# Kernel optimization log

Hardware: AMD Instinct MI355X
Metric: run time of the kernel (lower is better)

The kernel has to match this reference:

```python
import jax, jax.numpy as jnp
import numpy as np

N = 100000   # nodes
E = 800000   # directed edges (symmetrized to 2E in forward)
D0 = 128     # input feature dim (dim0)
H = 128      # hidden = h_dim * args.d = 64 * 2
L = 4        # num_layers
G = 64       # num graphs for global_mean_pool
BN_EPS = 1e-5
LN_EPS = 1e-5


def setup_inputs() -> dict:
    key = jax.random.key(0)
    ks = jax.random.split(key, 12)
    s = 1.0 / np.sqrt(H)
    x = jax.random.normal(ks[0], (N, D0), dtype=jnp.float32)
    row = jax.random.randint(ks[1], (E,), 0, N, dtype=jnp.int32)
    off = jax.random.randint(ks[2], (E,), 1, N, dtype=jnp.int32)
    col = (row + off) % N  # guarantees row != col (no self loops)
    edge_index = jnp.stack([row, col])
    batch = jnp.sort(jax.random.randint(ks[3], (N,), 0, G, dtype=jnp.int32))
    return {
        "x": x,
        "W0": jax.random.normal(ks[4], (D0, H), dtype=jnp.float32) * s,
        "b0": jnp.zeros((H,), jnp.float32),
        "eps_l": jnp.zeros((L,), jnp.float32),        # GIN eps per layer
        "W1": jax.random.normal(ks[5], (L, H, H), dtype=jnp.float32) * s,
        "b1": jnp.zeros((L, H), jnp.float32),
        "bn_g": jnp.ones((L, H), jnp.float32),
        "bn_b": jnp.zeros((L, H), jnp.float32),
        "W2": jax.random.normal(ks[6], (L, H, H), dtype=jnp.float32) * s,
        "b2": jnp.zeros((L, H), jnp.float32),
        "ln_g": jnp.ones((L, H), jnp.float32),
        "ln_b": jnp.zeros((L, H), jnp.float32),
        "edge_index": edge_index,
        "batch": batch,
    }


def reference(x, W0, b0, eps_l, W1, b1, bn_g, bn_b, W2, b2, ln_g, ln_b, edge_index, batch):
    n = x.shape[0]
    h = x @ W0 + b0  # layer0 encode -> [N, H]
    # FNSD: symmetrize edges (cat with flip) and drop self loops
    ei = jnp.concatenate([edge_index, edge_index[::-1]], axis=1)
    row, col = ei[0], ei[1]
    w = (row != col).astype(h.dtype)  # self-loop removal as zero edge weight
    for i in range(L):
        # GINConv: scatter-add of neighbor features
        agg = jax.ops.segment_sum(w[:, None] * h[col], row, num_segments=n)
        u = (1.0 + eps_l[i]) * h + agg
        # mlp: Linear -> BatchNorm1d (training-mode batch stats) -> ReLU -> Linear
        z = u @ W1[i] + b1[i]
        m = jnp.mean(z, axis=0)
        v = jnp.var(z, axis=0)
        z = (z - m) * jax.lax.rsqrt(v + BN_EPS) * bn_g[i] + bn_b[i]
        z = jax.nn.relu(z)
        z = z @ W2[i] + b2[i]
        z = jax.nn.relu(z)          # use_activation
        h = h + z                    # use_residual
        mu = jnp.mean(h, axis=-1, keepdims=True)   # LayerNorm
        var = jnp.var(h, axis=-1, keepdims=True)
        h = (h - mu) * jax.lax.rsqrt(var + LN_EPS) * ln_g[i] + ln_b[i]
    # global_mean_pool over graph ids
    cnt = jax.ops.segment_sum(jnp.ones((n,), h.dtype), batch, num_segments=G)
    sums = jax.ops.segment_sum(h, batch, num_segments=G)
    return sums / jnp.maximum(cnt, 1.0)[:, None]
```

## Files before the change

kernel.cpp:

```cpp
#include <hip/hip_runtime.h>

#define NN 100000
#define EE 800000
#define HH 128
#define LL 4
#define GG 64
#define BN_EPS 1e-5f
#define LN_EPS 1e-5f
#define POOL_CHUNK 64
#define NBUK ((NN + 255) >> 8)
#define CAP 8192
#define BCHUNK 8192

typedef __attribute__((ext_vector_type(8))) short short8;
typedef __attribute__((ext_vector_type(4))) float f32x4;

__device__ inline unsigned short bf16_rne(float f) {
    unsigned u = __float_as_uint(f);
    return (unsigned short)((u + 0x7FFF + ((u >> 16) & 1)) >> 16);
}
__device__ inline float bf16_to_f32(unsigned short h) {
    return __uint_as_float((unsigned)h << 16);
}


__global__ void setup_kernel(const float* __restrict__ W0, const float* __restrict__ W1,
                             const float* __restrict__ W2, short* __restrict__ wt_hi,
                             int* __restrict__ bcur, float* __restrict__ colsum,
                             float* __restrict__ psum, float* __restrict__ pcnt) {
    int i = blockIdx.x * 256 + threadIdx.x;
    if (i < NBUK) bcur[i] = i * CAP;
    if (i < LL * HH * 2) colsum[i] = 0.f;
    if (i < GG * HH) psum[i] = 0.f;
    if (i < GG) pcnt[i] = 0.f;
    if (i < 9 * HH * HH) {
        int mat = i >> 14, rem = i & 16383;
        int n = rem >> 7, k = rem & 127;
        const float* src = (mat == 0) ? W0 : ((mat <= 4) ? W1 + (size_t)(mat - 1) * HH * HH
                                                         : W2 + (size_t)(mat - 5) * HH * HH);
        float v = src[(size_t)k * HH + n];
        int off = (mat << 14) + (((k >> 3) * 8 + (n >> 4)) << 7) + ((n & 15) << 3) + (k & 7);
        wt_hi[off] = (short)bf16_rne(v);
    }
}


__global__ __launch_bounds__(256) void bucket_scatter(const int* __restrict__ ei, int* __restrict__ bcur,
                                                      int* __restrict__ pairs) {
    __shared__ int h[NBUK];
    __shared__ int curb[NBUK];
    int tid = threadIdx.x;
    for (int i = tid; i < NBUK; i += 256) h[i] = 0;
    __syncthreads();
    int base = blockIdx.x * BCHUNK;
#pragma unroll 4
    for (int k = 0; k < BCHUNK / 256; k++) {
        int e = base + k * 256 + tid;
        if (e < 2 * EE) {
            int r = ei[e];
            int c = (e < EE) ? ei[e + EE] : ei[e - EE];
            if (r != c) atomicAdd(&h[r >> 8], 1);
        }
    }
    __syncthreads();
    for (int i = tid; i < NBUK; i += 256) {
        int n = h[i];
        curb[i] = n ? atomicAdd(&bcur[i], n) : 0;
    }
    __syncthreads();
#pragma unroll 4
    for (int k = 0; k < BCHUNK / 256; k++) {
        int e = base + k * 256 + tid;
        if (e < 2 * EE) {
            int r = ei[e];
            int c = (e < EE) ? ei[e + EE] : ei[e - EE];
            if (r != c) {
                int p = atomicAdd(&curb[r >> 8], 1);
                pairs[p] = ((r & 255) << 17) | c;
            }
        }
    }
}

__global__ __launch_bounds__(256) void bucket_build(const int* __restrict__ pairs, const int* __restrict__ bcur,
                                                    int* __restrict__ rp, int* __restrict__ re,
                                                    int* __restrict__ colidx) {
    __shared__ int hist[256], off[256], lcol[CAP];
    int b = blockIdx.x, tid = threadIdx.x;
    int s = b * CAP;
    int size = bcur[b] - s;
    hist[tid] = 0;
    __syncthreads();
    for (int i = tid; i < size; i += 256) atomicAdd(&hist[pairs[s + i] >> 17], 1);
    __syncthreads();
    off[tid] = hist[tid];
    __syncthreads();
    for (int o = 1; o < 256; o <<= 1) {
        int x = (tid >= o) ? off[tid - o] : 0;
        __syncthreads();
        off[tid] += x;
        __syncthreads();
    }
    int excl = (tid > 0) ? off[tid - 1] : 0;
    int r = (b << 8) + tid;
    if (r < NN) { rp[r] = s + excl; re[r] = s + off[tid]; }
    hist[tid] = excl;
    __syncthreads();
    for (int i = tid; i < size; i += 256) {
        int u = pairs[s + i];
        int p = atomicAdd(&hist[u >> 17], 1);
        lcol[p] = u & 0x1FFFF;
    }
    __syncthreads();
    for (int i = tid; i < size; i += 256) colidx[s + i] = lcol[i];
}


__global__ __launch_bounds__(256) void agg_kernel(
    const unsigned int* __restrict__ hbf, const int* __restrict__ rp, const int* __restrict__ re,
    const int* __restrict__ colidx,
    const float* __restrict__ eps_l, int layer, float* __restrict__ u)
{
    int node = blockIdx.x * 4 + (threadIdx.x >> 6);
    if (node >= NN) return;
    int lane = threadIdx.x & 63;
    float eps1 = 1.0f + eps_l[layer];
    unsigned sv = hbf[node * 64 + lane];
    float ax = __uint_as_float(sv << 16) * eps1;
    float ay = __uint_as_float(sv & 0xFFFF0000u) * eps1;
    int i = rp[node], end = re[node];
    for (; i + 8 <= end; i += 8) {
        unsigned v[8];
#pragma unroll
        for (int j = 0; j < 8; j++) v[j] = hbf[colidx[i + j] * 64 + lane];
#pragma unroll
        for (int j = 0; j < 8; j++) {
            ax += __uint_as_float(v[j] << 16);
            ay += __uint_as_float(v[j] & 0xFFFF0000u);
        }
    }
    for (; i + 2 <= end; i += 2) {
        unsigned v0 = hbf[colidx[i] * 64 + lane];
        unsigned v1 = hbf[colidx[i + 1] * 64 + lane];
        ax += __uint_as_float(v0 << 16) + __uint_as_float(v1 << 16);
        ay += __uint_as_float(v0 & 0xFFFF0000u) + __uint_as_float(v1 & 0xFFFF0000u);
    }
    for (; i < end; i++) {
        unsigned v = hbf[colidx[i] * 64 + lane];
        ax += __uint_as_float(v << 16);
        ay += __uint_as_float(v & 0xFFFF0000u);
    }
    ((float2*)(u + (size_t)node * HH))[lane] = make_float2(ax, ay);
}


template<int MODE>
__global__ __launch_bounds__(256, 4) void gemm_v8(
    const void* __restrict__ Ain,
    const short* __restrict__ wt_hi,
    const float* __restrict__ bias,
    unsigned short* __restrict__ z1_out,
    float* __restrict__ colsum, float* __restrict__ colsq,
    const float* __restrict__ bng, const float* __restrict__ bnb,
    const float* __restrict__ lng, const float* __restrict__ lnb,
    unsigned short* __restrict__ hbf)
{
    __shared__ short wh[HH * HH];
    __shared__ float stats[2 * HH];
    int tid = threadIdx.x;
    int wave = tid >> 6, lane = tid & 63;
    int lrow = lane & 15, kgrp = lane >> 4;
    int r0 = blockIdx.x * 64;
    int arow = r0 + wave * 16 + lrow;

    {
        const short8* src = (const short8*)wt_hi;
        short8* dst = (short8*)wh;
#pragma unroll
        for (int i = 0; i < 8; i++) dst[tid + i * 256] = src[tid + i * 256];
    }
    if (MODE == 1) stats[tid] = 0.f;
    if (MODE == 2 && tid < HH) {
        float m = colsum[tid] * (1.f / NN);
        float v = colsq[tid] * (1.f / NN) - m * m;
        float a = bng[tid] * rsqrtf(v + BN_EPS);
        stats[tid] = a;
        stats[HH + tid] = bnb[tid] - m * a;
    }

    float4 a0[4], a1[4];
    short8 az[4];
    if (MODE == 2) {
        const unsigned short* Az = (const unsigned short*)Ain;
        if (arow < NN) {
#pragma unroll
            for (int ks = 0; ks < 4; ks++)
                az[ks] = *(const short8*)(Az + (size_t)arow * HH + ks * 32 + kgrp * 8);
        } else {
#pragma unroll
            for (int ks = 0; ks < 4; ks++) az[ks] = (short8){0,0,0,0,0,0,0,0};
        }
    } else {
        const float* Af = (const float*)Ain;
        if (arow < NN) {
#pragma unroll
            for (int ks = 0; ks < 4; ks++) {
                int kb = ks * 32 + kgrp * 8;
                a0[ks] = *(const float4*)(Af + (size_t)arow * HH + kb);
                a1[ks] = *(const float4*)(Af + (size_t)arow * HH + kb + 4);
            }
        } else {
#pragma unroll
            for (int ks = 0; ks < 4; ks++) {
                a0[ks] = make_float4(0.f, 0.f, 0.f, 0.f);
                a1[ks] = a0[ks];
            }
        }
    }
    __syncthreads();

    f32x4 acc[8];
#pragma unroll
    for (int c = 0; c < 8; c++) acc[c] = (f32x4){0.f, 0.f, 0.f, 0.f};

#pragma unroll
    for (int ks = 0; ks < 4; ks++) {
        int kb = ks * 32 + kgrp * 8;
        float av[8];
        if (MODE == 2) {
#pragma unroll
            for (int j = 0; j < 8; j++) {
                float zb = bf16_to_f32((unsigned short)az[ks][j]);
                av[j] = fmaxf(fmaf(zb, stats[kb + j], stats[HH + kb + j]), 0.f);
            }
        } else {
            av[0] = a0[ks].x; av[1] = a0[ks].y; av[2] = a0[ks].z; av[3] = a0[ks].w;
            av[4] = a1[ks].x; av[5] = a1[ks].y; av[6] = a1[ks].z; av[7] = a1[ks].w;
        }
        short8 ahi, alo;
#pragma unroll
        for (int j = 0; j < 8; j++) {
            unsigned short hb = bf16_rne(av[j]);
            ahi[j] = (short)hb;
            alo[j] = (short)bf16_rne(av[j] - bf16_to_f32(hb));
        }
        int fb = (ks * 4 + kgrp) * 8;
#pragma unroll
        for (int c = 0; c < 8; c++) {
            short8 whi = *(const short8*)(wh + ((fb + c) << 7) + (lrow << 3));
            acc[c] = __builtin_amdgcn_mfma_f32_16x16x32_bf16(ahi, whi, acc[c], 0, 0, 0);
            acc[c] = __builtin_amdgcn_mfma_f32_16x16x32_bf16(alo, whi, acc[c], 0, 0, 0);
        }
    }

    float bv[8];
#pragma unroll
    for (int c = 0; c < 8; c++) bv[c] = bias[c * 16 + lrow];
    int lrb = wave * 16 + kgrp * 4;
    unsigned short* hst = (unsigned short*)wh;

    if (MODE == 0) {
        __syncthreads();
#pragma unroll
        for (int c = 0; c < 8; c++)
#pragma unroll
            for (int reg = 0; reg < 4; reg++)
                hst[(lrb + reg) * HH + c * 16 + lrow] = bf16_rne(acc[c][reg] + bv[c]);
        __syncthreads();
#pragma unroll
        for (int i = 0; i < 4; i++) {
            int idx = tid + i * 256;
            int r = r0 + (idx >> 4);
            if (r < NN)
                *(uint4*)(hbf + (size_t)r * HH + (idx & 15) * 8) = ((const uint4*)wh)[idx];
        }
    } else if (MODE == 1) {
        __syncthreads();
        float ps[8], pq[8];
#pragma unroll
        for (int c = 0; c < 8; c++) { ps[c] = 0.f; pq[c] = 0.f; }
#pragma unroll
        for (int c = 0; c < 8; c++)
#pragma unroll
            for (int reg = 0; reg < 4; reg++) {
                float z = acc[c][reg] + bv[c];
                hst[(lrb + reg) * HH + c * 16 + lrow] = bf16_rne(z);
                if (r0 + lrb + reg < NN) { ps[c] += z; pq[c] += z * z; }
            }
#pragma unroll
        for (int c = 0; c < 8; c++) {
            ps[c] += __shfl_xor(ps[c], 16); pq[c] += __shfl_xor(pq[c], 16);
            ps[c] += __shfl_xor(ps[c], 32); pq[c] += __shfl_xor(pq[c], 32);
        }
        if (kgrp == 0) {
#pragma unroll
            for (int c = 0; c < 8; c++) {
                atomicAdd(&stats[c * 16 + lrow], ps[c]);
                atomicAdd(&stats[HH + c * 16 + lrow], pq[c]);
            }
        }
        __syncthreads();
#pragma unroll
        for (int i = 0; i < 4; i++) {
            int idx = tid + i * 256;
            int r = r0 + (idx >> 4);
            if (r < NN)
                *(uint4*)(z1_out + (size_t)r * HH + (idx & 15) * 8) = ((const uint4*)wh)[idx];
        }
        if (tid < HH) {
            atomicAdd(&colsum[tid], stats[tid]);
            atomicAdd(&colsq[tid], stats[HH + tid]);
        }
    } else {
        float lg[8], lb[8];
#pragma unroll
        for (int c = 0; c < 8; c++) {
            lg[c] = lng[c * 16 + lrow];
            lb[c] = lnb[c * 16 + lrow];
        }
        __syncthreads();
#pragma unroll
        for (int i = 0; i < 4; i++) {
            int idx = tid + i * 256;
            int r = r0 + (idx >> 4);
            uint4 v = make_uint4(0, 0, 0, 0);
            if (r < NN) v = *(const uint4*)(hbf + (size_t)r * HH + (idx & 15) * 8);
            ((uint4*)wh)[idx] = v;
        }
        __syncthreads();
#pragma unroll
        for (int reg = 0; reg < 4; reg++) {
            int r = r0 + lrb + reg;
            if (r < NN) {
                float tv[8];
                float s = 0.f, q = 0.f;
#pragma unroll
                for (int c = 0; c < 8; c++) {
                    float hold = bf16_to_f32(hst[(lrb + reg) * HH + c * 16 + lrow]);
                    tv[c] = hold + fmaxf(acc[c][reg] + bv[c], 0.f);
                    s += tv[c]; q += tv[c] * tv[c];
                }
#pragma unroll
                for (int m = 1; m < 16; m <<= 1) {
                    s += __shfl_xor(s, m);
                    q += __shfl_xor(q, m);
                }
                float mu = s * (1.f / 128.f);
                float var = q * (1.f / 128.f) - mu * mu;
                float rs = rsqrtf(var + LN_EPS);
#pragma unroll
                for (int c = 0; c < 8; c++)
                    hst[(lrb + reg) * HH + c * 16 + lrow] =
                        bf16_rne((tv[c] - mu) * rs * lg[c] + lb[c]);
            }
        }
        __syncthreads();
#pragma unroll
        for (int i = 0; i < 4; i++) {
            int idx = tid + i * 256;
            int r = r0 + (idx >> 4);
            if (r < NN)
                *(uint4*)(hbf + (size_t)r * HH + (idx & 15) * 8) = ((const uint4*)wh)[idx];
        }
    }
}


__global__ void pool_kernel(const unsigned short* __restrict__ h, const int* __restrict__ batch,
                            float* __restrict__ psum, float* __restrict__ pcnt)
{
    int t = threadIdx.x;
    int n0 = blockIdx.x * POOL_CHUNK;
    int n1 = n0 + POOL_CHUNK; if (n1 > NN) n1 = NN;
    if (n0 >= NN) return;
    float acc = 0.f;
    int cur = batch[n0];
    int cnt = 0;
    for (int n = n0; n < n1; n++) {
        int g = batch[n];
        if (g != cur) {
            atomicAdd(&psum[cur * HH + t], acc);
            if (t == 0) atomicAdd(&pcnt[cur], (float)cnt);
            acc = 0.f; cnt = 0; cur = g;
        }
        acc += bf16_to_f32(h[(size_t)n * HH + t]);
        cnt++;
    }
    atomicAdd(&psum[cur * HH + t], acc);
    if (t == 0) atomicAdd(&pcnt[cur], (float)cnt);
}

__global__ void pool_final(const float* __restrict__ psum, const float* __restrict__ pcnt,
                           float* __restrict__ out)
{
    int i = blockIdx.x * blockDim.x + threadIdx.x;
    if (i < GG * HH) {
        float c = pcnt[i >> 7];
        out[i] = psum[i] / fmaxf(c, 1.f);
    }
}


extern "C" void kernel_launch(void* const* d_in, const int* in_sizes, int n_in,
                              void* d_out, int out_size, void* d_ws, size_t ws_size,
                              hipStream_t stream)
{
    const float* x     = (const float*)d_in[0];
    const float* W0    = (const float*)d_in[1];
    const float* b0    = (const float*)d_in[2];
    const float* eps_l = (const float*)d_in[3];
    const float* W1    = (const float*)d_in[4];
    const float* b1    = (const float*)d_in[5];
    const float* bng   = (const float*)d_in[6];
    const float* bnb   = (const float*)d_in[7];
    const float* W2    = (const float*)d_in[8];
    const float* b2    = (const float*)d_in[9];
    const float* lng   = (const float*)d_in[10];
    const float* lnb   = (const float*)d_in[11];
    const int*   ei    = (const int*)d_in[12];
    const int*   batch = (const int*)d_in[13];
    float* out = (float*)d_out;

    char* ws = (char*)d_ws;
    size_t off = 0;
    auto alloc = [&](size_t bytes) -> void* {
        void* p = ws + off;
        off += (bytes + 255) & ~(size_t)255;
        return p;
    };
    unsigned short* hbf = (unsigned short*)alloc((size_t)NN * HH * 2);
    unsigned short* z1  = (unsigned short*)alloc((size_t)NN * HH * 2);
    float* ubuf   = (float*)alloc((size_t)NN * HH * 4);
    int*   colidx = (int*)alloc((size_t)NBUK * CAP * 4);
    int*   pairs  = (int*)alloc((size_t)NBUK * CAP * 4);
    int*   rp     = (int*)alloc((size_t)NN * 4);
    int*   re     = (int*)alloc((size_t)NN * 4);
    int*   bcur   = (int*)alloc((NBUK + 1) * 4);
    float* colsum = (float*)alloc((size_t)LL * HH * 2 * 4);
    float* psum   = (float*)alloc((size_t)GG * HH * 4);
    float* pcnt   = (float*)alloc(GG * 4);
    short* wt_hi  = (short*)alloc((size_t)9 * HH * HH * 2);

    setup_kernel<<<(9 * HH * HH + 255) / 256, 256, 0, stream>>>(W0, W1, W2, wt_hi, bcur,
                                                                colsum, psum, pcnt);

    bucket_scatter<<<(2 * EE + BCHUNK - 1) / BCHUNK, 256, 0, stream>>>(ei, bcur, pairs);
    bucket_build<<<NBUK, 256, 0, stream>>>(pairs, bcur, rp, re, colidx);

    int gb = (NN + 63) / 64;
    gemm_v8<0><<<gb, 256, 0, stream>>>(x, wt_hi, b0, nullptr,
                                       nullptr, nullptr, nullptr, nullptr, nullptr, nullptr, hbf);

    for (int l = 0; l < LL; l++) {
        float* cs = colsum + (size_t)l * HH * 2;
        float* cq = cs + HH;
        agg_kernel<<<(NN + 3) / 4, 256, 0, stream>>>((const unsigned*)hbf, rp, re, colidx,
                                                     eps_l, l, ubuf);
        gemm_v8<1><<<gb, 256, 0, stream>>>(ubuf, wt_hi + (size_t)(1 + l) * HH * HH,
                                           b1 + l * HH, z1,
                                           cs, cq, nullptr, nullptr, nullptr, nullptr, nullptr);
        gemm_v8<2><<<gb, 256, 0, stream>>>(z1, wt_hi + (size_t)(5 + l) * HH * HH,
                                           b2 + l * HH, nullptr,
                                           cs, cq, bng + l * HH, bnb + l * HH,
                                           lng + l * HH, lnb + l * HH, hbf);
    }

    pool_kernel<<<(NN + POOL_CHUNK - 1) / POOL_CHUNK, 128, 0, stream>>>(hbf, batch, psum, pcnt);
    pool_final<<<(GG * HH + 255) / 256, 256, 0, stream>>>(psum, pcnt, out);
}
```

Before: 725.8 us.

## Store aggregated features as bf16 and drop hi/lo split in first MLP GEMM

```diff
diff --git a/kernel.cpp b/kernel.cpp
--- a/kernel.cpp
+++ b/kernel.cpp
@@ -117,45 +117,46 @@
 
 
 __global__ __launch_bounds__(256) void agg_kernel(
-    const unsigned int* __restrict__ hbf, const int* __restrict__ rp, const int* __restrict__ re,
+    const uint2* __restrict__ hbf2, const int* __restrict__ rp, const int* __restrict__ re,
     const int* __restrict__ colidx,
-    const float* __restrict__ eps_l, int layer, float* __restrict__ u)
+    const float* __restrict__ eps_l, int layer, uint2* __restrict__ u2)
 {
-    int node = blockIdx.x * 4 + (threadIdx.x >> 6);
-    if (node >= NN) return;
     int lane = threadIdx.x & 63;
+    int half = lane >> 5, sub = lane & 31;
+    int node = blockIdx.x * 8 + (threadIdx.x >> 6) * 2 + half;
     float eps1 = 1.0f + eps_l[layer];
-    unsigned sv = hbf[node * 64 + lane];
-    float ax = __uint_as_float(sv << 16) * eps1;
-    float ay = __uint_as_float(sv & 0xFFFF0000u) * eps1;
-    int i = rp[node], end = re[node];
-    for (; i + 8 <= end; i += 8) {
-        unsigned v[8];
-#pragma unroll
-        for (int j = 0; j < 8; j++) v[j] = hbf[colidx[i + j] * 64 + lane];
+    uint2 sv = hbf2[(size_t)node * 32 + sub];
+    float a0 = bf16_to_f32((unsigned short)(sv.x & 0xFFFF)) * eps1;
+    float a1 = bf16_to_f32((unsigned short)(sv.x >> 16)) * eps1;
+    float a2 = bf16_to_f32((unsigned short)(sv.y & 0xFFFF)) * eps1;
+    float a3 = bf16_to_f32((unsigned short)(sv.y >> 16)) * eps1;
+    int base = rp[node];
+    int n = re[node] - base;
+    for (int i = 0; i < n; i += 8) {
+        uint2 v[8];
+        int c[8];
+#pragma unroll
+        for (int j = 0; j < 8; j++) c[j] = (i + j < n) ? colidx[base + i + j] : -1;
+#pragma unroll
+        for (int j = 0; j < 8; j++)
+            v[j] = (c[j] >= 0) ? hbf2[(size_t)c[j] * 32 + sub] : make_uint2(0u, 0u);
 #pragma unroll
         for (int j = 0; j < 8; j++) {
-            ax += __uint_as_float(v[j] << 16);
-            ay += __uint_as_float(v[j] & 0xFFFF0000u);
-        }
-    }
-    for (; i + 2 <= end; i += 2) {
-        unsigned v0 = hbf[colidx[i] * 64 + lane];
-        unsigned v1 = hbf[colidx[i + 1] * 64 + lane];
-        ax += __uint_as_float(v0 << 16) + __uint_as_float(v1 << 16);
-        ay += __uint_as_float(v0 & 0xFFFF0000u) + __uint_as_float(v1 & 0xFFFF0000u);
-    }
-    for (; i < end; i++) {
-        unsigned v = hbf[colidx[i] * 64 + lane];
-        ax += __uint_as_float(v << 16);
-        ay += __uint_as_float(v & 0xFFFF0000u);
-    }
-    ((float2*)(u + (size_t)node * HH))[lane] = make_float2(ax, ay);
+            a0 += bf16_to_f32((unsigned short)(v[j].x & 0xFFFF));
+            a1 += bf16_to_f32((unsigned short)(v[j].x >> 16));
+            a2 += bf16_to_f32((unsigned short)(v[j].y & 0xFFFF));
+            a3 += bf16_to_f32((unsigned short)(v[j].y >> 16));
+        }
+    }
+    uint2 o;
+    o.x = (unsigned)bf16_rne(a0) | ((unsigned)bf16_rne(a1) << 16);
+    o.y = (unsigned)bf16_rne(a2) | ((unsigned)bf16_rne(a3) << 16);
+    u2[(size_t)node * 32 + sub] = o;
 }
 
 
 template<int MODE>
-__global__ __launch_bounds__(256, 4) void gemm_v8(
+__global__ __launch_bounds__(256, 4) void gemm_v9(
     const void* __restrict__ Ain,
     const short* __restrict__ wt_hi,
     const float* __restrict__ bias,
@@ -190,7 +191,7 @@
 
     float4 a0[4], a1[4];
     short8 az[4];
-    if (MODE == 2) {
+    if (MODE != 0) {
         const unsigned short* Az = (const unsigned short*)Ain;
         if (arow < NN) {
 #pragma unroll
@@ -225,31 +226,39 @@
 
 #pragma unroll
     for (int ks = 0; ks < 4; ks++) {
-        int kb = ks * 32 + kgrp * 8;
-        float av[8];
-        if (MODE == 2) {
+        int fb = (ks * 4 + kgrp) * 8;
+        if (MODE == 1) {
+#pragma unroll
+            for (int c = 0; c < 8; c++) {
+                short8 whi = *(const short8*)(wh + ((fb + c) << 7) + (lrow << 3));
+                acc[c] = __builtin_amdgcn_mfma_f32_16x16x32_bf16(az[ks], whi, acc[c], 0, 0, 0);
+            }
+        } else {
+            int kb = ks * 32 + kgrp * 8;
+            float av[8];
+            if (MODE == 2) {
+#pragma unroll
+                for (int j = 0; j < 8; j++) {
+                    float zb = bf16_to_f32((unsigned short)az[ks][j]);
+                    av[j] = fmaxf(fmaf(zb, stats[kb + j], stats[HH + kb + j]), 0.f);
+                }
+            } else {
+                av[0] = a0[ks].x; av[1] = a0[ks].y; av[2] = a0[ks].z; av[3] = a0[ks].w;
+                av[4] = a1[ks].x; av[5] = a1[ks].y; av[6] = a1[ks].z; av[7] = a1[ks].w;
+            }
+            short8 ahi, alo;
 #pragma unroll
             for (int j = 0; j < 8; j++) {
-                float zb = bf16_to_f32((unsigned short)az[ks][j]);
-                av[j] = fmaxf(fmaf(zb, stats[kb + j], stats[HH + kb + j]), 0.f);
-            }
-        } else {
-            av[0] = a0[ks].x; av[1] = a0[ks].y; av[2] = a0[ks].z; av[3] = a0[ks].w;
-            av[4] = a1[ks].x; av[5] = a1[ks].y; av[6] = a1[ks].z; av[7] = a1[ks].w;
-        }
-        short8 ahi, alo;
-#pragma unroll
-        for (int j = 0; j < 8; j++) {
-            unsigned short hb = bf16_rne(av[j]);
-            ahi[j] = (short)hb;
-            alo[j] = (short)bf16_rne(av[j] - bf16_to_f32(hb));
-        }
-        int fb = (ks * 4 + kgrp) * 8;
-#pragma unroll
-        for (int c = 0; c < 8; c++) {
-            short8 whi = *(const short8*)(wh + ((fb + c) << 7) + (lrow << 3));
-            acc[c] = __builtin_amdgcn_mfma_f32_16x16x32_bf16(ahi, whi, acc[c], 0, 0, 0);
-            acc[c] = __builtin_amdgcn_mfma_f32_16x16x32_bf16(alo, whi, acc[c], 0, 0, 0);
+                unsigned short hb = bf16_rne(av[j]);
+                ahi[j] = (short)hb;
+                alo[j] = (short)bf16_rne(av[j] - bf16_to_f32(hb));
+            }
+#pragma unroll
+            for (int c = 0; c < 8; c++) {
+                short8 whi = *(const short8*)(wh + ((fb + c) << 7) + (lrow << 3));
+                acc[c] = __builtin_amdgcn_mfma_f32_16x16x32_bf16(ahi, whi, acc[c], 0, 0, 0);
+                acc[c] = __builtin_amdgcn_mfma_f32_16x16x32_bf16(alo, whi, acc[c], 0, 0, 0);
+            }
         }
     }
 
@@ -430,8 +439,8 @@
     };
     unsigned short* hbf = (unsigned short*)alloc((size_t)NN * HH * 2);
     unsigned short* z1  = (unsigned short*)alloc((size_t)NN * HH * 2);
-    float* ubuf   = (float*)alloc((size_t)NN * HH * 4);
-    int*   colidx = (int*)alloc((size_t)NBUK * CAP * 4);
+    unsigned short* ubuf = (unsigned short*)alloc((size_t)NN * HH * 2);
+    int*   colidx = (int*)alloc((size_t)NBUK * CAP * 4 + 1024);
     int*   pairs  = (int*)alloc((size_t)NBUK * CAP * 4);
     int*   rp     = (int*)alloc((size_t)NN * 4);
     int*   re     = (int*)alloc((size_t)NN * 4);
@@ -448,18 +457,18 @@
     bucket_build<<<NBUK, 256, 0, stream>>>(pairs, bcur, rp, re, colidx);
 
     int gb = (NN + 63) / 64;
-    gemm_v8<0><<<gb, 256, 0, stream>>>(x, wt_hi, b0, nullptr,
+    gemm_v9<0><<<gb, 256, 0, stream>>>(x, wt_hi, b0, nullptr,
                                        nullptr, nullptr, nullptr, nullptr, nullptr, nullptr, hbf);
 
     for (int l = 0; l < LL; l++) {
         float* cs = colsum + (size_t)l * HH * 2;
         float* cq = cs + HH;
-        agg_kernel<<<(NN + 3) / 4, 256, 0, stream>>>((const unsigned*)hbf, rp, re, colidx,
-                                                     eps_l, l, ubuf);
-        gemm_v8<1><<<gb, 256, 0, stream>>>(ubuf, wt_hi + (size_t)(1 + l) * HH * HH,
+        agg_kernel<<<NN / 8, 256, 0, stream>>>((const uint2*)hbf, rp, re, colidx,
+                                               eps_l, l, (uint2*)ubuf);
+        gemm_v9<1><<<gb, 256, 0, stream>>>(ubuf, wt_hi + (size_t)(1 + l) * HH * HH,
                                            b1 + l * HH, z1,
                                            cs, cq, nullptr, nullptr, nullptr, nullptr, nullptr);
-        gemm_v8<2><<<gb, 256, 0, stream>>>(z1, wt_hi + (size_t)(5 + l) * HH * HH,
+        gemm_v9<2><<<gb, 256, 0, stream>>>(z1, wt_hi + (size_t)(5 + l) * HH * HH,
                                            b2 + l * HH, nullptr,
                                            cs, cq, bng + l * HH, bnb + l * HH,
                                            lng + l * HH, lnb + l * HH, hbf);
```

Result: faster. 687.4 us (-5.3%).
